# Performance work log

Hardware: AMD Instinct MI355X
Metric: run time of the kernel (lower is better)

The kernel has to match this reference:

```python
import jax, jax.numpy as jnp
import numpy as np

WS = 5   # window_size
VN = 8   # view_num -> H = W = VN*WS = 40


def _layernorm(x, g, b, eps=1e-5):
    mu = x.mean(-1, keepdims=True)
    var = ((x - mu) ** 2).mean(-1, keepdims=True)
    return (x - mu) * jax.lax.rsqrt(var + eps) * g + b


def _rel_index():
    # standard Swin relative-position index for a WS x WS window
    coords = np.stack(np.meshgrid(np.arange(WS), np.arange(WS), indexing='ij')).reshape(2, -1)
    rel = (coords[:, :, None] - coords[:, None, :]).transpose(1, 2, 0)  # (T,T,2)
    rel = rel + (WS - 1)
    return rel[:, :, 0] * (2 * WS - 1) + rel[:, :, 1]  # (T,T) int


def _attn_mask(H, W):
    # checkerboard mask: outer product of flattened per-window checkerboard,
    # 0 where both positions are 'on', -100 elsewhere (matches masked_fill logic)
    ckbd = np.zeros((H, W), np.float32)
    ckbd[0::2, 1::2] = 1.0
    ckbd[1::2, 0::2] = 1.0
    win = ckbd.reshape(VN, WS, VN, WS).transpose(0, 2, 1, 3).reshape(VN * VN, WS * WS)
    m = win[:, :, None] * win[:, None, :]  # (N,T,T)
    return np.where(m == 0.0, -100.0, 0.0).astype(np.float32)


def setup_inputs() -> dict:
    key = jax.random.key(0)
    ks = jax.random.split(key, 8)
    B, C, H, W = 64, 256, 40, 40
    nh = 8
    dim2 = 2 * C
    hid = int(dim2 * 2.0)

    def n(k, shape, s=0.02):
        return jax.random.normal(k, shape, jnp.float32) * s

    return dict(
        x=jax.random.normal(ks[0], (B, C, H, W), jnp.float32),
        qkv_w=n(ks[1], (C, 3 * C)), qkv_b=jnp.zeros((3 * C,), jnp.float32),
        rel_table=n(ks[2], ((2 * WS - 1) ** 2, nh)),
        proj_w=n(ks[3], (C, dim2)), proj_b=jnp.zeros((dim2,), jnp.float32),
        mlp_w1=n(ks[4], (dim2, hid)), mlp_b1=jnp.zeros((hid,), jnp.float32),
        mlp_w2=n(ks[5], (hid, dim2)), mlp_b2=jnp.zeros((dim2,), jnp.float32),
        norm1_g=jnp.ones((C,), jnp.float32), norm1_b=jnp.zeros((C,), jnp.float32),
        norm2_g=jnp.ones((dim2,), jnp.float32), norm2_b=jnp.zeros((dim2,), jnp.float32),
    )


def reference(x, qkv_w, qkv_b, rel_table, proj_w, proj_b,
              mlp_w1, mlp_b1, mlp_w2, mlp_b2,
              norm1_g, norm1_b, norm2_g, norm2_b):
    B, C, H, W = x.shape
    nh = rel_table.shape[1]
    hd = C // nh
    N = VN * VN           # windows
    T = WS * WS           # tokens per window
    scale = hd ** -0.5

    xs = _layernorm(x.reshape(B, C, H * W).transpose(0, 2, 1), norm1_g, norm1_b)  # (B,L,C)
    qkv = xs @ qkv_w + qkv_b                                   # (B,L,3C)
    qkv = qkv.reshape(B, H, W, 3, C).transpose(3, 0, 4, 1, 2)  # (3,B,C,H,W)
    # windowize: (3,B,C,u,ws,v,ws) -> (3,B,N,C,T)
    qkv = qkv.reshape(3, B, C, VN, WS, VN, WS).transpose(0, 1, 3, 5, 2, 4, 6).reshape(3, B, N, C, T)
    # NOTE: original splits C as (head_dim, num_heads) -- head index is MINOR
    qkv = qkv.reshape(3, B, N, hd, nh, T).transpose(0, 1, 2, 4, 5, 3)  # (3,B,N,nh,T,hd)
    q, k, v = qkv[0] * scale, qkv[1], qkv[2]

    attn = jnp.einsum('bnhtd,bnhsd->bnhts', q, k)              # (B,N,nh,T,T)
    bias = rel_table[jnp.asarray(_rel_index())].transpose(2, 0, 1)  # (nh,T,T)
    mask = jnp.asarray(_attn_mask(H, W))                       # (N,T,T)
    attn = jax.nn.softmax(attn + bias[None, None] + mask[None, :, None], axis=-1)

    out = jnp.einsum('bnhts,bnhsd->bnhtd', attn, v)            # (B,N,nh,T,hd)
    out = out.reshape(B, N, nh, WS, WS, hd).transpose(0, 1, 3, 4, 2, 5)  # (B,N,ws,ws,nh,hd)
    # 'B (u v) h w nh c -> B (u h v w) (nh c)'
    out = out.reshape(B, VN, VN, WS, WS, C).transpose(0, 1, 3, 2, 4, 5).reshape(B, H * W, C)

    y = out @ proj_w + proj_b                                  # (B,L,2C)
    h = _layernorm(y, norm2_g, norm2_b)
    h = jax.nn.gelu(h @ mlp_w1 + mlp_b1, approximate=False) @ mlp_w2 + mlp_b2
    y = y + h
    return y.transpose(0, 2, 1).reshape(B, -1, H, W)           # (B,2C,H,W)
```

## Files before the change

kernel.cpp:

```cpp
#include <hip/hip_runtime.h>
#include <math.h>

#define B_   64
#define C_   256
#define L_   1600
#define T_   25
#define ROWS (B_*L_)
#define QSCALE 0.17677669529663687f

typedef _Float16 f16;
typedef f16 f16x8 __attribute__((ext_vector_type(8)));
typedef f16 f16x4 __attribute__((ext_vector_type(4)));
typedef f16 f16x2 __attribute__((ext_vector_type(2)));
typedef float f32x4 __attribute__((ext_vector_type(4)));

__device__ __forceinline__ void gload_lds16(const void* g, void* l) {
  __builtin_amdgcn_global_load_lds(
      (const __attribute__((address_space(1))) unsigned int*)g,
      (__attribute__((address_space(3))) unsigned int*)l, 16, 0, 0);
}

__device__ __forceinline__ float dot8(f16x8 a, f16x8 b, float acc) {
  union U { f16x8 v; f16x2 p[4]; };
  U ua; ua.v = a;
  U ub; ub.v = b;
#pragma unroll
  for (int i = 0; i < 4; ++i)
    acc = __builtin_amdgcn_fdot2(ua.p[i], ub.p[i], acc, false);
  return acc;
}

__global__ __launch_bounds__(256) void wtrans_all(
    const float* __restrict__ wq, const float* __restrict__ wp,
    const float* __restrict__ wm1, const float* __restrict__ wm2,
    f16* __restrict__ oq, f16* __restrict__ op,
    f16* __restrict__ om1, f16* __restrict__ om2) {
  int bid = blockIdx.x;
  const float* w; f16* o; int K, N, nb, idx;
  if (bid < 48)       { w = wq;  o = oq;  K = 256;  N = 768;  idx = bid;       nb = 12; }
  else if (bid < 80)  { w = wp;  o = op;  K = 256;  N = 512;  idx = bid - 48;  nb = 8;  }
  else if (bid < 208) { w = wm1; o = om1; K = 512;  N = 1024; idx = bid - 80;  nb = 16; }
  else                { w = wm2; o = om2; K = 1024; N = 512;  idx = bid - 208; nb = 8;  }
  int n0 = (idx % nb) * 64, k0 = (idx / nb) * 64;

  __shared__ f16 tile[64][72];
  int tid = threadIdx.x;
  int nn = tid & 63, kq = tid >> 6;
#pragma unroll
  for (int i = 0; i < 16; ++i) {
    int k = kq * 16 + i;
    tile[nn][k] = (f16)w[(size_t)(k0 + k) * N + n0 + nn];
  }
  __syncthreads();
#pragma unroll
  for (int jj = 0; jj < 2; ++jj) {
    int e = jj * 256 + tid;
    int nr = e >> 3, kb = e & 7;
    *(f16x8*)&o[(size_t)(n0 + nr) * K + k0 + kb * 8] = *(const f16x8*)&tile[nr][kb * 8];
  }
}

__global__ __launch_bounds__(256) void ln1_fused(const float* __restrict__ x,
    const float* __restrict__ g, const float* __restrict__ be,
    f16* __restrict__ xs) {
  __shared__ float t32[256][65];
  __shared__ float gL[256], beL[256];
  int tid = threadIdx.x;
  gL[tid] = g[tid]; beL[tid] = be[tid];
  int r0 = blockIdx.x * 64;
  int w = tid >> 6, rl = tid & 63;
  int grow = r0 + rl;
  int b = grow / L_, l = grow - b * L_;
  const float* xb = x + (size_t)b * (C_ * L_) + l;
#pragma unroll
  for (int i = 0; i < 64; ++i) {
    int c = w + i * 4;
    t32[c][rl] = xb[(size_t)c * L_];
  }
  __syncthreads();
  int row = tid >> 2, q = tid & 3;
  float s = 0.f, s2 = 0.f;
#pragma unroll
  for (int i = 0; i < 64; ++i) {
    int ii = (i + q * 8) & 63;
    float vv = t32[q * 64 + ii][row];
    s += vv; s2 += vv * vv;
  }
  s += __shfl_xor(s, 1); s2 += __shfl_xor(s2, 1);
  s += __shfl_xor(s, 2); s2 += __shfl_xor(s2, 2);
  float m = s * (1.0f / 256.0f);
  float rr = rsqrtf(s2 * (1.0f / 256.0f) - m * m + 1e-5f);
  f16* orow = &xs[(size_t)(r0 + row) * 256 + q * 64];
#pragma unroll
  for (int z8 = 0; z8 < 8; ++z8) {
    int zb = (z8 + q * 2) & 7;
    f16x8 ov;
#pragma unroll
    for (int z = 0; z < 8; ++z) {
      int c = q * 64 + zb * 8 + z;
      ov[z] = (f16)((t32[c][row] - m) * rr * gL[c] + beL[c]);
    }
    *(f16x8*)(orow + zb * 8) = ov;
  }
}

template<int K, int N, int EPI, int NCB>
__global__ __launch_bounds__(256) void gemm16(
    const f16* __restrict__ A, const f16* __restrict__ BT,
    const float* __restrict__ bias,
    float* __restrict__ outF, f16* __restrict__ outH,
    const f16* __restrict__ resid, int row_off, int nrp8) {
  __shared__ f16 As[3][128 * 32];
  __shared__ f16 Bs[3][128 * 32];
  int tid = threadIdx.x;
  int w = tid >> 6, lane = tid & 63;
  int wr = w >> 1, wc = w & 1;
  int bid = blockIdx.x;
  int xcd = bid & 7, j1d = bid >> 3;
  int member = j1d % NCB, grp = j1d / NCB;
  int r0 = (xcd * nrp8 + grp) * 128;
  int n0 = member * 128;

  f32x4 acc[4][4] = {};

  int srow0 = w * 16 + (lane >> 2);
  int st4 = lane & 3;

  const int NT = K / 32;

#define STAGE_T(kt, bi)                                                       \
  {                                                                           \
    int k0s = (kt) * 32;                                                      \
    _Pragma("unroll")                                                         \
    for (int i = 0; i < 2; ++i) {                                             \
      int row = i * 64 + srow0;                                               \
      int cb = st4 ^ ((row >> 1) & 3);                                        \
      gload_lds16(A + (size_t)(r0 + row) * K + k0s + cb * 8,                  \
                  &As[bi][(i * 4 + w) * 512]);                                \
    }                                                                         \
    _Pragma("unroll")                                                         \
    for (int i = 0; i < 2; ++i) {                                             \
      int row = i * 64 + srow0;                                               \
      int cb = st4 ^ ((row >> 1) & 3);                                        \
      gload_lds16(BT + (size_t)(n0 + row) * K + k0s + cb * 8,                 \
                  &Bs[bi][(i * 4 + w) * 512]);                                \
    }                                                                         \
  }

#define COMPUTE_T(bi)                                                         \
  {                                                                           \
    f16x8 af[4], bf[4];                                                       \
    _Pragma("unroll")                                                         \
    for (int m = 0; m < 4; ++m) {                                             \
      int ar = wr * 64 + m * 16 + (lane & 15);                                \
      int sl = (lane >> 4) ^ ((ar >> 1) & 3);                                 \
      af[m] = *(const f16x8*)&As[bi][ar * 32 + sl * 8];                       \
    }                                                                         \
    _Pragma("unroll")                                                         \
    for (int n = 0; n < 4; ++n) {                                             \
      int br = wc * 64 + n * 16 + (lane & 15);                                \
      int sl = (lane >> 4) ^ ((br >> 1) & 3);                                 \
      bf[n] = *(const f16x8*)&Bs[bi][br * 32 + sl * 8];                       \
    }                                                                         \
    __builtin_amdgcn_s_setprio(1);                                            \
    _Pragma("unroll")                                                         \
    for (int m = 0; m < 4; ++m)                                               \
      _Pragma("unroll")                                                       \
      for (int n = 0; n < 4; ++n)                                             \
        acc[m][n] =                                                           \
            __builtin_amdgcn_mfma_f32_16x16x32_f16(af[m], bf[n], acc[m][n],   \
                                                   0, 0, 0);                  \
    __builtin_amdgcn_s_setprio(0);                                            \
  }

  STAGE_T(0, 0);
  STAGE_T(1, 1);

  for (int t = 0; t < NT - 1; ++t) {
    asm volatile("s_waitcnt vmcnt(4)" ::: "memory");
    __builtin_amdgcn_s_barrier();
    COMPUTE_T(t % 3);
    if (t + 2 < NT) STAGE_T(t + 2, (t + 2) % 3);
  }
  asm volatile("s_waitcnt vmcnt(0)" ::: "memory");
  __builtin_amdgcn_s_barrier();
  COMPUTE_T((NT - 1) % 3);

#undef STAGE_T
#undef COMPUTE_T

  if constexpr (EPI != 3) {
#pragma unroll
    for (int m = 0; m < 4; ++m) {
#pragma unroll
      for (int n = 0; n < 4; ++n) {
        int gcol = n0 + wc * 64 + n * 16 + (lane & 15);
        float bb = bias[gcol];
#pragma unroll
        for (int j = 0; j < 4; ++j) {
          int grow = r0 + wr * 64 + m * 16 + ((lane >> 4) << 2) + j;
          float vv = acc[m][n][j] + bb;
          if constexpr (EPI == 0) {
            outH[(size_t)grow * N + gcol] = (f16)vv;
          } else {
            float z = 0.7978845608028654f * (vv + 0.044715f * vv * vv * vv);
            float e2 = __expf(2.0f * z);
            float th = 1.0f - 2.0f / (e2 + 1.0f);
            float gl = 0.5f * vv * (1.0f + th);
            outH[(size_t)grow * N + gcol] = (f16)gl;
          }
        }
      }
    }
  } else {
#pragma unroll
    for (int m = 0; m < 4; ++m) {
      int growl = r0 + wr * 64 + m * 16 + ((lane >> 4) << 2);
      int growg = row_off + growl;
      int b = growg / L_;
      int l = growg - b * L_;
#pragma unroll
      for (int n = 0; n < 4; ++n) {
        int gcol = n0 + wc * 64 + n * 16 + (lane & 15);
        float bb = bias[gcol];
        float4 o;
        o.x = acc[m][n][0] + bb + (float)resid[(size_t)(growg + 0) * 512 + gcol];
        o.y = acc[m][n][1] + bb + (float)resid[(size_t)(growg + 1) * 512 + gcol];
        o.z = acc[m][n][2] + bb + (float)resid[(size_t)(growg + 2) * 512 + gcol];
        o.w = acc[m][n][3] + bb + (float)resid[(size_t)(growg + 3) * 512 + gcol];
        *(float4*)&outF[((size_t)b * 512 + gcol) * L_ + l] = o;
      }
    }
  }
}

#define PST 776
__global__ __launch_bounds__(512) void attn_kernel(const f16* __restrict__ qkv,
                                                   const float* __restrict__ rel,
                                                   f16* __restrict__ outp) {
  __shared__ f16 qc[2][T_][PST];
  __shared__ f16 relL[81 * 8];
  int tid = threadIdx.x;
  int wl = tid >> 8;
  int tl = tid & 255;
  int bn = blockIdx.x * 2 + wl;
  int b = bn >> 6, n = bn & 63;
  int u = n >> 3, v = n & 7;

  for (int e = tid; e < 648; e += 512) relL[e] = (f16)rel[e];

  for (int e = tl; e < T_ * 96; e += 256) {
    int t = e / 96;
    int g = e - t * 96;
    int i = t / 5, j = t - i * 5;
    int l = (u * 5 + i) * 40 + v * 5 + j;
    f16x8 val = *(const f16x8*)&qkv[(size_t)(b * L_ + l) * 768 + g * 8];
    int which = g >> 5;
    int d = g & 31;
    int base = which * 256 + d;
#pragma unroll
    for (int h = 0; h < 8; ++h)
      qc[wl][t][base + h * 32] = val[h];
  }
  __syncthreads();

  int h = tl >> 5, t = tl & 31;
  if (t < T_) {
    int i1 = t / 5, j1 = t - i1 * 5;
    int par1 = (u + v + i1 + j1) & 1;
    const f16* qp = &qc[wl][t][h * 32];
    f16x8 q0 = *(const f16x8*)(qp + 0);
    f16x8 q1 = *(const f16x8*)(qp + 8);
    f16x8 q2 = *(const f16x8*)(qp + 16);
    f16x8 q3 = *(const f16x8*)(qp + 24);

    float p[T_];
    float mx = -1e30f;
#pragma unroll
    for (int s = 0; s < T_; ++s) {
      int i2 = s / 5, j2 = s - i2 * 5;
      const f16* kp = &qc[wl][s][256 + h * 32];
      f16x8 k0 = *(const f16x8*)(kp + 0);
      f16x8 k1 = *(const f16x8*)(kp + 8);
      f16x8 k2 = *(const f16x8*)(kp + 16);
      f16x8 k3 = *(const f16x8*)(kp + 24);
      float d0 = 0.f, d1 = 0.f;
      d0 = dot8(q0, k0, d0);
      d1 = dot8(q1, k1, d1);
      d0 = dot8(q2, k2, d0);
      d1 = dot8(q3, k3, d1);
      float bias = (float)relL[((i1 - i2 + 4) * 9 + (j1 - j2 + 4)) * 8 + h];
      int par2 = (u + v + i2 + j2) & 1;
      float sc = (d0 + d1) * QSCALE + bias + ((par1 & par2) ? 0.0f : -100.0f);
      p[s] = sc;
      mx = fmaxf(mx, sc);
    }
    float sum = 0.f;
#pragma unroll
    for (int s = 0; s < T_; ++s) {
      float e = __expf(p[s] - mx);
      p[s] = e;
      sum += e;
    }
    float inv = 1.0f / sum;
#pragma unroll
    for (int s = 0; s < T_; ++s) p[s] *= inv;

    int l = (u * 5 + i1) * 40 + v * 5 + j1;
    f16* op = &outp[(size_t)(b * L_ + l) * 256 + h * 32];

    f16x2 acc2[16];
#pragma unroll
    for (int k = 0; k < 16; ++k) { acc2[k][0] = (f16)0.f; acc2[k][1] = (f16)0.f; }
#pragma unroll
    for (int s = 0; s < T_; ++s) {
      const f16* vp = &qc[wl][s][512 + h * 32];
      union VU { f16x8 v8; f16x2 v2[4]; };
      VU v0, v1, v2q, v3;
      v0.v8  = *(const f16x8*)(vp + 0);
      v1.v8  = *(const f16x8*)(vp + 8);
      v2q.v8 = *(const f16x8*)(vp + 16);
      v3.v8  = *(const f16x8*)(vp + 24);
      f16 ps = (f16)p[s];
      f16x2 pp; pp[0] = ps; pp[1] = ps;
#pragma unroll
      for (int k = 0; k < 4; ++k) {
        acc2[k]      += pp * v0.v2[k];
        acc2[4 + k]  += pp * v1.v2[k];
        acc2[8 + k]  += pp * v2q.v2[k];
        acc2[12 + k] += pp * v3.v2[k];
      }
    }
#pragma unroll
    for (int z8 = 0; z8 < 4; ++z8) {
      union VU { f16x8 v8; f16x2 v2[4]; };
      VU ov;
#pragma unroll
      for (int k = 0; k < 4; ++k) ov.v2[k] = acc2[z8 * 4 + k];
      *(f16x8*)(op + z8 * 8) = ov.v8;
    }
  }
}

__global__ __launch_bounds__(256) void ln2_fused(const f16* __restrict__ y,
    const float* __restrict__ g, const float* __restrict__ be,
    f16* __restrict__ yln) {
  int wv = threadIdx.x >> 6, lane = threadIdx.x & 63;
  int row = blockIdx.x * 4 + wv;
  const f16x8* yp = (const f16x8*)(y + (size_t)row * 512);
  f16x8 h0 = yp[lane];
  float v[8];
  float s = 0.f, s2 = 0.f;
#pragma unroll
  for (int z = 0; z < 8; ++z) {
    v[z] = (float)h0[z];
    s += v[z]; s2 += v[z] * v[z];
  }
#pragma unroll
  for (int o = 32; o; o >>= 1) { s += __shfl_xor(s, o); s2 += __shfl_xor(s2, o); }
  float m = s * (1.0f / 512.0f);
  float rr = rsqrtf(s2 * (1.0f / 512.0f) - m * m + 1e-5f);
  float4 g0 = ((const float4*)g)[lane * 2], g1 = ((const float4*)g)[lane * 2 + 1];
  float4 b0 = ((const float4*)be)[lane * 2], b1 = ((const float4*)be)[lane * 2 + 1];
  float gg[8] = {g0.x, g0.y, g0.z, g0.w, g1.x, g1.y, g1.z, g1.w};
  float bb[8] = {b0.x, b0.y, b0.z, b0.w, b1.x, b1.y, b1.z, b1.w};
  f16x8 o8;
#pragma unroll
  for (int z = 0; z < 8; ++z)
    o8[z] = (f16)((v[z] - m) * rr * gg[z] + bb[z]);
  *(f16x8*)&yln[(size_t)row * 512 + lane * 8] = o8;
}

extern "C" void kernel_launch(void* const* d_in, const int* in_sizes, int n_in,
                              void* d_out, int out_size, void* d_ws, size_t ws_size,
                              hipStream_t stream) {
  const float* x      = (const float*)d_in[0];
  const float* qkv_w  = (const float*)d_in[1];
  const float* qkv_b  = (const float*)d_in[2];
  const float* rel    = (const float*)d_in[3];
  const float* proj_w = (const float*)d_in[4];
  const float* proj_b = (const float*)d_in[5];
  const float* w1     = (const float*)d_in[6];
  const float* b1     = (const float*)d_in[7];
  const float* w2     = (const float*)d_in[8];
  const float* b2     = (const float*)d_in[9];
  const float* g1     = (const float*)d_in[10];
  const float* be1    = (const float*)d_in[11];
  const float* g2     = (const float*)d_in[12];
  const float* be2    = (const float*)d_in[13];
  float* out = (float*)d_out;

  char* w8 = (char*)d_ws;
  f16* qkv_wT  = (f16*)(w8 + 1638400);
  f16* proj_wT = qkv_wT + 768 * 256;
  f16* w1T     = proj_wT + 512 * 256;
  f16* w2T     = w1T + 1024 * 512;
  char* P0 = w8 + 4390912;
  f16* qkv_h = (f16*)P0;
  f16* y_h   = (f16*)P0;
  char* P1 = P0 + (size_t)ROWS * 768 * 2;
  f16* xs_h  = (f16*)P1;
  f16* att_h = (f16*)(P1 + (size_t)ROWS * 256 * 2);
  f16* yln   = (f16*)P1;
  char* P2 = P1 + (size_t)ROWS * 512 * 2;
  f16* hid = (f16*)P2;

  size_t need_full = 4390912 + (size_t)ROWS * 768 * 2 + (size_t)ROWS * 512 * 2
                   + (size_t)ROWS * 1024 * 2;
  bool full = ws_size >= need_full;

  wtrans_all<<<336, 256, 0, stream>>>(qkv_w, proj_w, w1, w2,
                                      qkv_wT, proj_wT, w1T, w2T);

  ln1_fused<<<ROWS / 64, 256, 0, stream>>>(x, g1, be1, xs_h);

  gemm16<256, 768, 0, 6><<<6 * (ROWS / 128), 256, 0, stream>>>(
      xs_h, qkv_wT, qkv_b, nullptr, qkv_h, nullptr, 0, (ROWS / 128) / 8);

  attn_kernel<<<B_ * 32, 512, 0, stream>>>(qkv_h, rel, att_h);

  gemm16<256, 512, 0, 4><<<4 * (ROWS / 128), 256, 0, stream>>>(
      att_h, proj_wT, proj_b, nullptr, y_h, nullptr, 0, (ROWS / 128) / 8);

  ln2_fused<<<ROWS / 4, 256, 0, stream>>>(y_h, g2, be2, yln);

  if (full) {
    gemm16<512, 1024, 2, 8><<<8 * (ROWS / 128), 256, 0, stream>>>(
        yln, w1T, b1, nullptr, hid, nullptr, 0, (ROWS / 128) / 8);
    gemm16<1024, 512, 3, 4><<<4 * (ROWS / 128), 256, 0, stream>>>(
        hid, w2T, b2, out, nullptr, y_h, 0, (ROWS / 128) / 8);
  } else {
    const int CHUNK = ROWS / 4;
    for (int c = 0; c < 4; ++c) {
      int off = c * CHUNK;
      gemm16<512, 1024, 2, 8><<<8 * (CHUNK / 128), 256, 0, stream>>>(
          yln + (size_t)off * 512, w1T, b1, nullptr, hid, nullptr, off, (CHUNK / 128) / 8);
      gemm16<1024, 512, 3, 4><<<4 * (CHUNK / 128), 256, 0, stream>>>(
          hid, w2T, b2, out, nullptr, y_h, off, (CHUNK / 128) / 8);
    }
  }
  (void)in_sizes; (void)n_in; (void)out_size;
}
```

Baseline: 652.6 us.

## Fold LayerNorm2 affine into MLP1 weights and apply row stats in epilogue

Replaces the materialized LN2 output with a stats-only kernel that writes per-row mean and rstd, folds gamma into the transposed W1 weights, and precomputes the column sums of gamma*W1 and the folded bias beta*W1+b1. The MLP1 GEMM now reads the raw projection output and applies rstd*(acc - mean*gsum) + bias in its epilogue. This removes the full write and re-read of the normalized activation tensor, at the cost of an extra small prep kernel and some precision risk, since centering now happens after the fp16 GEMM accumulation (cancellation).

```diff
diff --git a/kernel.cpp b/kernel.cpp
--- a/kernel.cpp
+++ b/kernel.cpp
@@ -33,13 +33,14 @@
 __global__ __launch_bounds__(256) void wtrans_all(
     const float* __restrict__ wq, const float* __restrict__ wp,
     const float* __restrict__ wm1, const float* __restrict__ wm2,
+    const float* __restrict__ g2,
     f16* __restrict__ oq, f16* __restrict__ op,
     f16* __restrict__ om1, f16* __restrict__ om2) {
   int bid = blockIdx.x;
-  const float* w; f16* o; int K, N, nb, idx;
+  const float* w; f16* o; int K, N, nb, idx; bool scale = false;
   if (bid < 48)       { w = wq;  o = oq;  K = 256;  N = 768;  idx = bid;       nb = 12; }
   else if (bid < 80)  { w = wp;  o = op;  K = 256;  N = 512;  idx = bid - 48;  nb = 8;  }
-  else if (bid < 208) { w = wm1; o = om1; K = 512;  N = 1024; idx = bid - 80;  nb = 16; }
+  else if (bid < 208) { w = wm1; o = om1; K = 512;  N = 1024; idx = bid - 80;  nb = 16; scale = true; }
   else                { w = wm2; o = om2; K = 1024; N = 512;  idx = bid - 208; nb = 8;  }
   int n0 = (idx % nb) * 64, k0 = (idx / nb) * 64;
 
@@ -49,7 +50,8 @@
 #pragma unroll
   for (int i = 0; i < 16; ++i) {
     int k = kq * 16 + i;
-    tile[nn][k] = (f16)w[(size_t)(k0 + k) * N + n0 + nn];
+    float sc = scale ? g2[k0 + k] : 1.0f;
+    tile[nn][k] = (f16)(w[(size_t)(k0 + k) * N + n0 + nn] * sc);
   }
   __syncthreads();
 #pragma unroll
@@ -58,6 +60,21 @@
     int nr = e >> 3, kb = e & 7;
     *(f16x8*)&o[(size_t)(n0 + nr) * K + k0 + kb * 8] = *(const f16x8*)&tile[nr][kb * 8];
   }
+}
+
+__global__ __launch_bounds__(256) void gprep(const float* __restrict__ w1,
+    const float* __restrict__ g2, const float* __restrict__ be2,
+    const float* __restrict__ b1,
+    float* __restrict__ gsum, float* __restrict__ bc) {
+  int n = blockIdx.x * 256 + threadIdx.x;
+  float sg = 0.f, sb = 0.f;
+  for (int c = 0; c < 512; ++c) {
+    float w = w1[(size_t)c * 1024 + n];
+    sg += g2[c] * w;
+    sb += be2[c] * w;
+  }
+  gsum[n] = sg;
+  bc[n] = sb + b1[n];
 }
 
 __global__ __launch_bounds__(256) void ln1_fused(const float* __restrict__ x,
@@ -109,7 +126,8 @@
     const f16* __restrict__ A, const f16* __restrict__ BT,
     const float* __restrict__ bias,
     float* __restrict__ outF, f16* __restrict__ outH,
-    const f16* __restrict__ resid, int row_off, int nrp8) {
+    const f16* __restrict__ resid, int row_off, int nrp8,
+    const float2* __restrict__ murs, const float* __restrict__ gsum) {
   __shared__ f16 As[3][128 * 32];
   __shared__ f16 Bs[3][128 * 32];
   int tid = threadIdx.x;
@@ -189,7 +207,7 @@
 #undef STAGE_T
 #undef COMPUTE_T
 
-  if constexpr (EPI != 3) {
+  if constexpr (EPI == 0) {
 #pragma unroll
     for (int m = 0; m < 4; ++m) {
 #pragma unroll
@@ -199,16 +217,31 @@
 #pragma unroll
         for (int j = 0; j < 4; ++j) {
           int grow = r0 + wr * 64 + m * 16 + ((lane >> 4) << 2) + j;
-          float vv = acc[m][n][j] + bb;
-          if constexpr (EPI == 0) {
-            outH[(size_t)grow * N + gcol] = (f16)vv;
-          } else {
-            float z = 0.7978845608028654f * (vv + 0.044715f * vv * vv * vv);
-            float e2 = __expf(2.0f * z);
-            float th = 1.0f - 2.0f / (e2 + 1.0f);
-            float gl = 0.5f * vv * (1.0f + th);
-            outH[(size_t)grow * N + gcol] = (f16)gl;
-          }
+          outH[(size_t)grow * N + gcol] = (f16)(acc[m][n][j] + bb);
+        }
+      }
+    }
+  } else if constexpr (EPI == 2) {
+#pragma unroll
+    for (int m = 0; m < 4; ++m) {
+      float2 mr[4];
+#pragma unroll
+      for (int j = 0; j < 4; ++j)
+        mr[j] = murs[row_off + r0 + wr * 64 + m * 16 + ((lane >> 4) << 2) + j];
+#pragma unroll
+      for (int n = 0; n < 4; ++n) {
+        int gcol = n0 + wc * 64 + n * 16 + (lane & 15);
+        float bcv = bias[gcol];
+        float gs = gsum[gcol];
+#pragma unroll
+        for (int j = 0; j < 4; ++j) {
+          int grow = r0 + wr * 64 + m * 16 + ((lane >> 4) << 2) + j;
+          float vv = mr[j].y * (acc[m][n][j] - mr[j].x * gs) + bcv;
+          float z = 0.7978845608028654f * (vv + 0.044715f * vv * vv * vv);
+          float e2 = __expf(2.0f * z);
+          float th = 1.0f - 2.0f / (e2 + 1.0f);
+          float gl = 0.5f * vv * (1.0f + th);
+          outH[(size_t)grow * N + gcol] = (f16)gl;
         }
       }
     }
@@ -342,33 +375,24 @@
   }
 }
 
-__global__ __launch_bounds__(256) void ln2_fused(const f16* __restrict__ y,
-    const float* __restrict__ g, const float* __restrict__ be,
-    f16* __restrict__ yln) {
+__global__ __launch_bounds__(256) void ln2_stats(const f16* __restrict__ y,
+                                                 float2* __restrict__ murs) {
   int wv = threadIdx.x >> 6, lane = threadIdx.x & 63;
   int row = blockIdx.x * 4 + wv;
-  const f16x8* yp = (const f16x8*)(y + (size_t)row * 512);
-  f16x8 h0 = yp[lane];
-  float v[8];
+  f16x8 h0 = *(const f16x8*)(y + (size_t)row * 512 + lane * 8);
   float s = 0.f, s2 = 0.f;
 #pragma unroll
   for (int z = 0; z < 8; ++z) {
-    v[z] = (float)h0[z];
-    s += v[z]; s2 += v[z] * v[z];
+    float v = (float)h0[z];
+    s += v; s2 += v * v;
   }
 #pragma unroll
   for (int o = 32; o; o >>= 1) { s += __shfl_xor(s, o); s2 += __shfl_xor(s2, o); }
-  float m = s * (1.0f / 512.0f);
-  float rr = rsqrtf(s2 * (1.0f / 512.0f) - m * m + 1e-5f);
-  float4 g0 = ((const float4*)g)[lane * 2], g1 = ((const float4*)g)[lane * 2 + 1];
-  float4 b0 = ((const float4*)be)[lane * 2], b1 = ((const float4*)be)[lane * 2 + 1];
-  float gg[8] = {g0.x, g0.y, g0.z, g0.w, g1.x, g1.y, g1.z, g1.w};
-  float bb[8] = {b0.x, b0.y, b0.z, b0.w, b1.x, b1.y, b1.z, b1.w};
-  f16x8 o8;
-#pragma unroll
-  for (int z = 0; z < 8; ++z)
-    o8[z] = (f16)((v[z] - m) * rr * gg[z] + bb[z]);
-  *(f16x8*)&yln[(size_t)row * 512 + lane * 8] = o8;
+  if (lane == 0) {
+    float m = s * (1.0f / 512.0f);
+    float rr = rsqrtf(s2 * (1.0f / 512.0f) - m * m + 1e-5f);
+    murs[row] = make_float2(m, rr);
+  }
 }
 
 extern "C" void kernel_launch(void* const* d_in, const int* in_sizes, int n_in,
@@ -391,6 +415,9 @@
   float* out = (float*)d_out;
 
   char* w8 = (char*)d_ws;
+  float2* murs = (float2*)w8;
+  float* gsum  = (float*)(w8 + 819200);
+  float* bc    = gsum + 1024;
   f16* qkv_wT  = (f16*)(w8 + 1638400);
   f16* proj_wT = qkv_wT + 768 * 256;
   f16* w1T     = proj_wT + 512 * 256;
@@ -401,7 +428,6 @@
   char* P1 = P0 + (size_t)ROWS * 768 * 2;
   f16* xs_h  = (f16*)P1;
   f16* att_h = (f16*)(P1 + (size_t)ROWS * 256 * 2);
-  f16* yln   = (f16*)P1;
   char* P2 = P1 + (size_t)ROWS * 512 * 2;
   f16* hid = (f16*)P2;
 
@@ -409,34 +435,41 @@
                    + (size_t)ROWS * 1024 * 2;
   bool full = ws_size >= need_full;
 
-  wtrans_all<<<336, 256, 0, stream>>>(qkv_w, proj_w, w1, w2,
+  wtrans_all<<<336, 256, 0, stream>>>(qkv_w, proj_w, w1, w2, g2,
                                       qkv_wT, proj_wT, w1T, w2T);
+  gprep<<<4, 256, 0, stream>>>(w1, g2, be2, b1, gsum, bc);
 
   ln1_fused<<<ROWS / 64, 256, 0, stream>>>(x, g1, be1, xs_h);
 
   gemm16<256, 768, 0, 6><<<6 * (ROWS / 128), 256, 0, stream>>>(
-      xs_h, qkv_wT, qkv_b, nullptr, qkv_h, nullptr, 0, (ROWS / 128) / 8);
+      xs_h, qkv_wT, qkv_b, nullptr, qkv_h, nullptr, 0, (ROWS / 128) / 8,
+      nullptr, nullptr);
 
   attn_kernel<<<B_ * 32, 512, 0, stream>>>(qkv_h, rel, att_h);
 
   gemm16<256, 512, 0, 4><<<4 * (ROWS / 128), 256, 0, stream>>>(
-      att_h, proj_wT, proj_b, nullptr, y_h, nullptr, 0, (ROWS / 128) / 8);
-
-  ln2_fused<<<ROWS / 4, 256, 0, stream>>>(y_h, g2, be2, yln);
+      att_h, proj_wT, proj_b, nullptr, y_h, nullptr, 0, (ROWS / 128) / 8,
+      nullptr, nullptr);
+
+  ln2_stats<<<ROWS / 4, 256, 0, stream>>>(y_h, murs);
 
   if (full) {
     gemm16<512, 1024, 2, 8><<<8 * (ROWS / 128), 256, 0, stream>>>(
-        yln, w1T, b1, nullptr, hid, nullptr, 0, (ROWS / 128) / 8);
+        y_h, w1T, bc, nullptr, hid, nullptr, 0, (ROWS / 128) / 8,
+        murs, gsum);
     gemm16<1024, 512, 3, 4><<<4 * (ROWS / 128), 256, 0, stream>>>(
-        hid, w2T, b2, out, nullptr, y_h, 0, (ROWS / 128) / 8);
+        hid, w2T, b2, out, nullptr, y_h, 0, (ROWS / 128) / 8,
+        nullptr, nullptr);
   } else {
     const int CHUNK = ROWS / 4;
     for (int c = 0; c < 4; ++c) {
       int off = c * CHUNK;
       gemm16<512, 1024, 2, 8><<<8 * (CHUNK / 128), 256, 0, stream>>>(
-          yln + (size_t)off * 512, w1T, b1, nullptr, hid, nullptr, off, (CHUNK / 128) / 8);
+          y_h + (size_t)off * 512, w1T, bc, nullptr, hid, nullptr, off, (CHUNK / 128) / 8,
+          murs, gsum);
       gemm16<1024, 512, 3, 4><<<4 * (CHUNK / 128), 256, 0, stream>>>(
-          hid, w2T, b2, out, nullptr, y_h, off, (CHUNK / 128) / 8);
+          hid, w2T, b2, out, nullptr, y_h, off, (CHUNK / 128) / 8,
+          nullptr, nullptr);
     }
   }
   (void)in_sizes; (void)n_in; (void)out_size;
```

Result: slower. 666.7 us (+2.2%).
